# Kernel optimization log

Hardware: AMD Instinct MI355X
Metric: run time of the kernel (lower is better)

The kernel has to match this reference:

```python
import jax, jax.numpy as jnp
import numpy as np


def setup_inputs() -> dict:
    key = jax.random.key(0)
    k1, k2, k3 = jax.random.split(key, 3)
    B, C, L, D = 2, 8, 256, 128
    start_hidden = jax.random.normal(k1, (B, C, L, D), dtype=jnp.float32)
    end_hidden = jax.random.normal(k2, (B, C, L, D), dtype=jnp.float32)
    # nn.Parameter initialized uniform_(-0.1, 0.1)
    v = jax.random.uniform(k3, (D,), dtype=jnp.float32, minval=-0.1, maxval=0.1)
    return {"start_hidden": start_hidden, "end_hidden": end_hidden, "v": v}


def reference(start_hidden, end_hidden, v):
    # start_hidden: [B, C, L, D], end_hidden: [B, C, L, D], v: [D]
    # additive pairwise scoring: tanh(s_i + e_j) . v  for every (i, j) span
    add_hidden = jnp.tanh(start_hidden[:, :, :, None, :] + end_hidden[:, :, None, :, :])  # [B,C,L,L,D]
    res = jnp.einsum('bcnmd,d->bcnm', add_hidden, v)  # [B, C, L, L]
    span_ner_mat_tensor = jnp.transpose(res, (0, 2, 3, 1))  # [B, L, L, C]
    return span_ner_mat_tensor
```

## Files before the change

### kernel.cpp

```cpp
#include <hip/hip_runtime.h>


#define LDIM 256
#define DDIM 128
#define DPAD 132

__device__ __forceinline__ float quad_term(const float4 s, const float4 e,
                                           float v0, float v1, float v2, float v3) {
    float p0 = s.x * e.x, p1 = s.y * e.y, p2 = s.z * e.z, p3 = s.w * e.w;
    float a = p0 + 1.0f, b = p1 + 1.0f, c = p2 + 1.0f, d = p3 + 1.0f;
    float n01 = fmaf(v1, a, v0 * b);
    float n23 = fmaf(v3, c, v2 * d);
    float r01 = __builtin_amdgcn_rcpf(a * b);
    float r23 = __builtin_amdgcn_rcpf(c * d);
    return fmaf(n01, r01, n23 * r23);
}

__global__ __launch_bounds__(256) void span_tanh_dot_kernel(
    const float* __restrict__ start_h,
    const float* __restrict__ end_h,
    const float* __restrict__ v,
    float* __restrict__ out,
    int C)
{
    __shared__ float s_t[32][DPAD];
    __shared__ float e_t[32][DPAD];
    __shared__ float s_vsum;

    const int bc = blockIdx.z;
    const int i0 = blockIdx.y * 32;
    const int j0 = blockIdx.x * 32;
    const int tx = threadIdx.x;
    const int ty = threadIdx.y;
    const int tid = ty * 16 + tx;

    const float K = 2.8853900817779268f;

    const float* sg = start_h + ((size_t)bc * LDIM + i0) * DDIM;
    const float* eg = end_h   + ((size_t)bc * LDIM + j0) * DDIM;

    #pragma unroll
    for (int idx = tid; idx < 32 * 32; idx += 256) {
        const int r  = idx >> 5;
        const int c4 = (idx & 31) << 2;
        float4 a = *(const float4*)(sg + r * DDIM + c4);
        a.x = __builtin_amdgcn_exp2f(K * a.x);
        a.y = __builtin_amdgcn_exp2f(K * a.y);
        a.z = __builtin_amdgcn_exp2f(K * a.z);
        a.w = __builtin_amdgcn_exp2f(K * a.w);
        *(float4*)(&s_t[r][c4]) = a;
        float4 b = *(const float4*)(eg + r * DDIM + c4);
        b.x = __builtin_amdgcn_exp2f(K * b.x);
        b.y = __builtin_amdgcn_exp2f(K * b.y);
        b.z = __builtin_amdgcn_exp2f(K * b.z);
        b.w = __builtin_amdgcn_exp2f(K * b.w);
        *(float4*)(&e_t[r][c4]) = b;
    }

    if (tid < 64) {
        float2 vv = *(const float2*)(v + 2 * tid);
        float p = vv.x + vv.y;
        #pragma unroll
        for (int off = 32; off > 0; off >>= 1) p += __shfl_down(p, off);
        if (tid == 0) s_vsum = p;
    }
    __syncthreads();

    const float* s0 = &s_t[ty][0];
    const float* s1 = &s_t[ty + 16][0];
    const float* e0 = &e_t[tx][0];
    const float* e1 = &e_t[tx + 16][0];

    float acc00 = 0.f, acc01 = 0.f, acc10 = 0.f, acc11 = 0.f;

    #pragma unroll 4
    for (int d = 0; d < DDIM; d += 4) {
        const float4 sa = *(const float4*)(s0 + d);
        const float4 sb = *(const float4*)(s1 + d);
        const float4 ea = *(const float4*)(e0 + d);
        const float4 eb = *(const float4*)(e1 + d);
        const float v0 = v[d], v1 = v[d + 1], v2 = v[d + 2], v3 = v[d + 3];

        acc00 += quad_term(sa, ea, v0, v1, v2, v3);
        acc01 += quad_term(sa, eb, v0, v1, v2, v3);
        acc10 += quad_term(sb, ea, v0, v1, v2, v3);
        acc11 += quad_term(sb, eb, v0, v1, v2, v3);
    }

    const int b = bc / C;
    const int c = bc - b * C;
    const float S = s_vsum;
    const int ia = i0 + ty, ib = i0 + ty + 16;
    const int ja = j0 + tx, jb = j0 + tx + 16;
    const size_t base = ((size_t)b * LDIM) * LDIM * C + c;

    out[base + ((size_t)ia * LDIM + ja) * C] = fmaf(-2.f, acc00, S);
    out[base + ((size_t)ia * LDIM + jb) * C] = fmaf(-2.f, acc01, S);
    out[base + ((size_t)ib * LDIM + ja) * C] = fmaf(-2.f, acc10, S);
    out[base + ((size_t)ib * LDIM + jb) * C] = fmaf(-2.f, acc11, S);
}

extern "C" void kernel_launch(void* const* d_in, const int* in_sizes, int n_in,
                              void* d_out, int out_size, void* d_ws, size_t ws_size,
                              hipStream_t stream) {
    const float* start_h = (const float*)d_in[0];
    const float* end_h   = (const float*)d_in[1];
    const float* v       = (const float*)d_in[2];
    float* out = (float*)d_out;

    const int BC = in_sizes[0] / (LDIM * DDIM);
    const int C  = 8;

    dim3 grid(LDIM / 32, LDIM / 32, BC);
    dim3 block(16, 16);
    span_tanh_dot_kernel<<<grid, block, 0, stream>>>(start_h, end_h, v, out, C);
}
```

Before: 21.10 us.

## Enlarge tile to 64x64 with 4x4 register blocking and restructured rational tanh sum

Each block now covers a 64x64 (i,j) tile and each thread computes a 4x4 micro-tile, so every LDS float4 load is reused across four partners instead of two. The per-term arithmetic is also restructured: the four-element group is combined into a single numerator over one reciprocal, using fmaf for the +1 terms, which halves the rcp count. In exchange the grid drops from 1024 to 256 blocks, which may underfill the GPU's CUs, while LDS use (~67KB) and register pressure both rise. Folding four terms into one denominator also risks overflow or precision loss for large exp values.

```diff
diff --git a/kernel.cpp b/kernel.cpp
--- a/kernel.cpp
+++ b/kernel.cpp
@@ -4,17 +4,6 @@
 #define LDIM 256
 #define DDIM 128
 #define DPAD 132
-
-__device__ __forceinline__ float quad_term(const float4 s, const float4 e,
-                                           float v0, float v1, float v2, float v3) {
-    float p0 = s.x * e.x, p1 = s.y * e.y, p2 = s.z * e.z, p3 = s.w * e.w;
-    float a = p0 + 1.0f, b = p1 + 1.0f, c = p2 + 1.0f, d = p3 + 1.0f;
-    float n01 = fmaf(v1, a, v0 * b);
-    float n23 = fmaf(v3, c, v2 * d);
-    float r01 = __builtin_amdgcn_rcpf(a * b);
-    float r23 = __builtin_amdgcn_rcpf(c * d);
-    return fmaf(n01, r01, n23 * r23);
-}
 
 __global__ __launch_bounds__(256) void span_tanh_dot_kernel(
     const float* __restrict__ start_h,
@@ -23,13 +12,13 @@
     float* __restrict__ out,
     int C)
 {
-    __shared__ float s_t[32][DPAD];
-    __shared__ float e_t[32][DPAD];
+    __shared__ float s_t[64][DPAD];
+    __shared__ float e_t[64][DPAD];
     __shared__ float s_vsum;
 
     const int bc = blockIdx.z;
-    const int i0 = blockIdx.y * 32;
-    const int j0 = blockIdx.x * 32;
+    const int i0 = blockIdx.y * 64;
+    const int j0 = blockIdx.x * 64;
     const int tx = threadIdx.x;
     const int ty = threadIdx.y;
     const int tid = ty * 16 + tx;
@@ -40,7 +29,8 @@
     const float* eg = end_h   + ((size_t)bc * LDIM + j0) * DDIM;
 
     #pragma unroll
-    for (int idx = tid; idx < 32 * 32; idx += 256) {
+    for (int k = 0; k < 8; ++k) {
+        const int idx = tid + k * 256;
         const int r  = idx >> 5;
         const int c4 = (idx & 31) << 2;
         float4 a = *(const float4*)(sg + r * DDIM + c4);
@@ -66,38 +56,56 @@
     }
     __syncthreads();
 
-    const float* s0 = &s_t[ty][0];
-    const float* s1 = &s_t[ty + 16][0];
-    const float* e0 = &e_t[tx][0];
-    const float* e1 = &e_t[tx + 16][0];
-
-    float acc00 = 0.f, acc01 = 0.f, acc10 = 0.f, acc11 = 0.f;
+    float acc[4][4];
+    #pragma unroll
+    for (int a = 0; a < 4; ++a)
+        #pragma unroll
+        for (int b = 0; b < 4; ++b) acc[a][b] = 0.0f;
 
     #pragma unroll 4
     for (int d = 0; d < DDIM; d += 4) {
-        const float4 sa = *(const float4*)(s0 + d);
-        const float4 sb = *(const float4*)(s1 + d);
-        const float4 ea = *(const float4*)(e0 + d);
-        const float4 eb = *(const float4*)(e1 + d);
+        float4 S[4], E[4];
+        S[0] = *(const float4*)(&s_t[ty     ][d]);
+        S[1] = *(const float4*)(&s_t[ty + 16][d]);
+        S[2] = *(const float4*)(&s_t[ty + 32][d]);
+        S[3] = *(const float4*)(&s_t[ty + 48][d]);
+        E[0] = *(const float4*)(&e_t[tx     ][d]);
+        E[1] = *(const float4*)(&e_t[tx + 16][d]);
+        E[2] = *(const float4*)(&e_t[tx + 32][d]);
+        E[3] = *(const float4*)(&e_t[tx + 48][d]);
         const float v0 = v[d], v1 = v[d + 1], v2 = v[d + 2], v3 = v[d + 3];
 
-        acc00 += quad_term(sa, ea, v0, v1, v2, v3);
-        acc01 += quad_term(sa, eb, v0, v1, v2, v3);
-        acc10 += quad_term(sb, ea, v0, v1, v2, v3);
-        acc11 += quad_term(sb, eb, v0, v1, v2, v3);
+        #pragma unroll
+        for (int a = 0; a < 4; ++a) {
+            #pragma unroll
+            for (int b = 0; b < 4; ++b) {
+                float qa = fmaf(S[a].x, E[b].x, 1.0f);
+                float qb = fmaf(S[a].y, E[b].y, 1.0f);
+                float qc = fmaf(S[a].z, E[b].z, 1.0f);
+                float qd = fmaf(S[a].w, E[b].w, 1.0f);
+                float ab = qa * qb, cd = qc * qd;
+                float n01 = fmaf(v0, qb, v1 * qa);
+                float n23 = fmaf(v2, qd, v3 * qc);
+                float N = fmaf(n01, cd, n23 * ab);
+                float r = __builtin_amdgcn_rcpf(ab * cd);
+                acc[a][b] = fmaf(N, r, acc[a][b]);
+            }
+        }
     }
 
-    const int b = bc / C;
-    const int c = bc - b * C;
-    const float S = s_vsum;
-    const int ia = i0 + ty, ib = i0 + ty + 16;
-    const int ja = j0 + tx, jb = j0 + tx + 16;
-    const size_t base = ((size_t)b * LDIM) * LDIM * C + c;
-
-    out[base + ((size_t)ia * LDIM + ja) * C] = fmaf(-2.f, acc00, S);
-    out[base + ((size_t)ia * LDIM + jb) * C] = fmaf(-2.f, acc01, S);
-    out[base + ((size_t)ib * LDIM + ja) * C] = fmaf(-2.f, acc10, S);
-    out[base + ((size_t)ib * LDIM + jb) * C] = fmaf(-2.f, acc11, S);
+    const int b_ = bc / C;
+    const int c_ = bc - b_ * C;
+    const float Sv = s_vsum;
+    #pragma unroll
+    for (int a = 0; a < 4; ++a) {
+        const int i = i0 + ty + 16 * a;
+        #pragma unroll
+        for (int b2 = 0; b2 < 4; ++b2) {
+            const int j = j0 + tx + 16 * b2;
+            out[(((size_t)b_ * LDIM + i) * LDIM + j) * C + c_] =
+                fmaf(-2.0f, acc[a][b2], Sv);
+        }
+    }
 }
 
 extern "C" void kernel_launch(void* const* d_in, const int* in_sizes, int n_in,
@@ -111,7 +119,7 @@
     const int BC = in_sizes[0] / (LDIM * DDIM);
     const int C  = 8;
 
-    dim3 grid(LDIM / 32, LDIM / 32, BC);
+    dim3 grid(LDIM / 64, LDIM / 64, BC);
     dim3 block(16, 16);
     span_tanh_dot_kernel<<<grid, block, 0, stream>>>(start_h, end_h, v, out, C);
 }
```

New measurement: 23.77 us. 1.13x slower.
